# Kernel optimization log

Hardware: AMD Instinct MI355X
Metric: run time of the kernel (lower is better)

## Reference

```python
import jax, jax.numpy as jnp
from jax import lax
import numpy as np

B = 8
IN_SCALE = 9            # 1 + 2*input_window_size
S2 = IN_SCALE * IN_SCALE  # 81
MODES = 16
J = 5 * S2 + MODES      # 421
RBF = 64
HDC = 256
NCA_H = 32
NCA_STEPS = 20
MAX_T = 100.0           # max_time_step (None in source -> bug; fixed constant)


def _pool_matrix(I, O):
    # faithful AdaptiveAvgPool over dim of size I -> O (torch bin boundaries)
    M = np.zeros((O, I), np.float32)
    for o in range(O):
        s = (o * I) // O
        e = -((-(o + 1) * I) // O)
        M[o, s:e] = 1.0 / (e - s)
    return jnp.asarray(M)

POOL = _pool_matrix(J, S2)  # [81, 421]


def _meta_encoding(m_in, m_out):
    # vectorized version of the per-i loop in meta_encoding
    pos_in = m_in / MAX_T
    pos_out = m_out / MAX_T
    i = jnp.arange(MODES)
    div = jnp.power(10000.0, (2.0 * (i // 2)).astype(jnp.float32) / MODES)
    a_in = pos_in[:, None] / div[None, :]   # [B, MODES]
    a_out = pos_out[:, None] / div[None, :]
    even = (jnp.sin(a_in) + jnp.cos(a_in)) * 0.5
    odd = (jnp.cos(a_in) + jnp.sin(a_out)) * 0.5
    return jnp.where((i % 2 == 0)[None, :], even, odd)


def setup_inputs() -> dict:
    key = jax.random.key(0)
    ks = jax.random.split(key, 12)
    data_input = jax.random.uniform(ks[0], (B, 4 * IN_SCALE, IN_SCALE), jnp.float32)
    structure_input = jax.random.uniform(ks[1], (B, IN_SCALE, IN_SCALE), jnp.float32)
    meta_in = jax.random.uniform(ks[2], (B,), jnp.float32) * MAX_T
    meta_out = jax.random.uniform(ks[3], (B,), jnp.float32) * MAX_T
    # learned / fixed params
    rbf_probes = jax.random.uniform(ks[4], (RBF, J, HDC), jnp.float32) * 2.0
    compress_w = jax.random.normal(ks[5], (5, RBF), jnp.float32)
    compress_b = jnp.full((5,), 0.01, jnp.float32)
    nca_w1 = jax.random.normal(ks[6], (NCA_H, 5, 3, 3), jnp.float32) * 0.1
    nca_b1 = jnp.full((NCA_H,), 0.01, jnp.float32)
    nca_w2 = jax.random.normal(ks[7], (5, NCA_H), jnp.float32) * 0.1
    nca_b2 = jnp.full((5,), 0.01, jnp.float32)
    # sparse random +/-1 HDC projection matrix (scatter into flat zeros, as in source)
    input_dim = 5 * S2
    n_nz = input_dim * HDC
    idx = np.asarray(jax.random.randint(ks[8], (n_nz,), 0, input_dim * HDC))
    signs = np.asarray(jax.random.randint(ks[9], (n_nz,), 0, 2)).astype(np.float32) * 2.0 - 1.0
    flat = np.zeros((B * J * HDC,), np.float32)
    flat[idx] = signs
    hdc_matrix = jnp.asarray(flat.reshape(B, J, HDC))
    return {
        "data_input": data_input, "structure_input": structure_input,
        "meta_in": meta_in, "meta_out": meta_out,
        "rbf_probes": rbf_probes, "hdc_matrix": hdc_matrix,
        "compress_w": compress_w, "compress_b": compress_b,
        "nca_w1": nca_w1, "nca_b1": nca_b1, "nca_w2": nca_w2, "nca_b2": nca_b2,
    }


def _forward(data_input, structure_input, meta_in, meta_out, rbf_probes,
             hdc_matrix, compress_w, compress_b, nca_w1, nca_b1, nca_w2, nca_b2):
    pe = _meta_encoding(meta_in, meta_out)                       # [B, 16]
    data = jnp.concatenate(
        [data_input.reshape(B, -1), structure_input.reshape(B, -1), pe], axis=1)  # [B, J]
    # einsum 'bi,bjd->bjd' sums data over i and broadcasts over (j, d)
    proj = data.sum(axis=1)[:, None, None] * hdc_matrix          # [B, J, HDC]
    # broadcast RBF distance: the big memory-bound intermediate [B, RBF, J, HDC]
    dist = (rbf_probes[None, :, :, :] - proj[:, None, :, :]) ** 2
    # 1x1 conv over rbf channel dim, then tanh -> [B, 5, J, HDC]
    x = jnp.tanh(jnp.einsum('brjd,or->bojd', dist, compress_w)
                 + compress_b[None, :, None, None])

    def nca_step(x, _):
        h = lax.conv_general_dilated(x, nca_w1, (1, 1), 'SAME',
                                     dimension_numbers=('NCHW', 'OIHW', 'NCHW'))
        h = jax.nn.relu(h + nca_b1[None, :, None, None])
        dx = jnp.einsum('bhjd,oh->bojd', h, nca_w2) + nca_b2[None, :, None, None]
        return x + dx, None

    x, _ = lax.scan(nca_step, x, None, length=NCA_STEPS)
    x = jnp.tanh(x)
    # AdaptiveAvgPool2d((S2, 1)): mean over HDC, adaptive pool J -> S2
    x = jnp.einsum('bcj,oj->bco', x.mean(axis=-1), POOL)         # [B, 5, 81]
    r = x[:, 0, :].reshape(B, IN_SCALE, IN_SCALE)
    g = x[:, 1, :].reshape(B, IN_SCALE, IN_SCALE)
    b = x[:, 2, :].reshape(B, IN_SCALE, IN_SCALE)
    a = x[:, 3, :].reshape(B, IN_SCALE, IN_SCALE)
    s = x[:, 4, :].reshape(B, IN_SCALE, IN_SCALE)
    return (r, g, b, a, s)


def reference(data_input, structure_input, meta_in, meta_out, rbf_probes,
              hdc_matrix, compress_w, compress_b, nca_w1, nca_b1, nca_w2, nca_b2):
    return _forward(data_input, structure_input, meta_in, meta_out, rbf_probes,
                    hdc_matrix, compress_w, compress_b, nca_w1, nca_b1, nca_w2, nca_b2)
```

## Files before the change

### kernel.cpp

```cpp
#include <hip/hip_runtime.h>
#include <math.h>

#define NB 8
#define JJ 421
#define HDCN 256
#define PP (JJ*HDCN)
#define STEPS 20

typedef __attribute__((ext_vector_type(8))) short bf16x8;
typedef __attribute__((ext_vector_type(4))) float f32x4;
typedef __attribute__((ext_vector_type(2))) float f32x2;
typedef __attribute__((ext_vector_type(4))) unsigned int uint4v;
typedef __attribute__((ext_vector_type(2))) int int2v;
typedef unsigned short ushort;
typedef unsigned int uint;

__device__ __forceinline__ ushort f2bf(float f) {
    union { float f; uint u; } a; a.f = f;
    uint r = 0x7fffu + ((a.u >> 16) & 1u);
    return (ushort)((a.u + r) >> 16);
}
__device__ __forceinline__ uint splitpack(float x) {
    uint u = __float_as_uint(x);
    uint r = 0x7fffu + ((u >> 16) & 1u);
    uint hib = (u + r) & 0xffff0000u;
    float lo = x - __uint_as_float(hib);
    return hib | f2bf(lo);
}
__device__ __forceinline__ float unpack2(uint p) {
    return __uint_as_float(p & 0xffff0000u) + __uint_as_float(p << 16);
}
__device__ __forceinline__ float tanh_fast(float x) {
    float e = __expf(2.f * x);
    return 1.f - 2.f / (e + 1.f);
}
__device__ __forceinline__ float wave_reduce_sum(float v) {
#pragma unroll
    for (int off = 32; off > 0; off >>= 1) v += __shfl_down(v, off);
    return v;
}
__device__ __forceinline__ float red32(float d) {
#if __has_builtin(__builtin_amdgcn_permlane32_swap)
    int2v pr = __builtin_amdgcn_permlane32_swap(__float_as_int(d), __float_as_int(d), false, false);
    return __int_as_float(pr.x) + __int_as_float(pr.y);
#else
    return d + __shfl_xor(d, 32);
#endif
}

__global__ __launch_bounds__(256) void k_wprep(
    const float* __restrict__ w1, const float* __restrict__ b1,
    const float* __restrict__ w2,
    ushort* __restrict__ Pw, float* __restrict__ w2p)
{
    int t = threadIdx.x;
    for (int idx = t; idx < 3072; idx += 256) {
        int p = idx >> 10, rem = idx & 1023, oc = rem >> 5, k = rem & 31;
        int tau = k & 15;
        float v = 0.f;
        if (tau < 15) v = w1[oc * 45 + (tau / 3) * 9 + (tau % 3) * 3 + p];
        Pw[idx] = f2bf(v);
    }
    int oc = t >> 3, o = t & 7;
    float v = 0.f;
    if (o < 5) v = w2[o * 32 + oc];
    else if (o == 5) v = b1[oc];
    w2p[t] = v;
}

__global__ __launch_bounds__(128) void k_prep(
    const float* __restrict__ din, const float* __restrict__ stin,
    const float* __restrict__ m_in, const float* __restrict__ m_out,
    float* __restrict__ sbuf)
{
    int b = blockIdx.x, t = threadIdx.x;
    float acc = 0.f;
    for (int k = t; k < 324; k += 128) acc += din[b * 324 + k];
    for (int k = t; k < 81;  k += 128) acc += stin[b * 81 + k];
    if (t < 16) {
        int i = t;
        float pos_in  = m_in[b]  * 0.01f;
        float pos_out = m_out[b] * 0.01f;
        float div = powf(10000.0f, (float)(2 * (i / 2)) / 16.0f);
        float ai = pos_in / div, ao = pos_out / div;
        float v = ((i & 1) == 0) ? 0.5f * (sinf(ai) + cosf(ai))
                                 : 0.5f * (cosf(ai) + sinf(ao));
        acc += v;
    }
    __shared__ float part[2];
    float w = wave_reduce_sum(acc);
    if ((t & 63) == 0) part[t >> 6] = w;
    __syncthreads();
    if (t == 0) sbuf[b] = part[0] + part[1];
}

__global__ __launch_bounds__(128) void k_x0(
    const float* __restrict__ rbf, const float* __restrict__ hdc,
    const float* __restrict__ cw, const float* __restrict__ cb,
    const float* __restrict__ sbuf, uint* __restrict__ x0)
{
    __shared__ float wl[320];
    __shared__ float Cw[5];
    __shared__ float sb[8];
    __shared__ float cbs[5];
    int t = threadIdx.x;
    for (int k = t; k < 320; k += 128) wl[k] = cw[k];
    if (t < 8)   sb[t] = sbuf[t];
    if (t < 5)   cbs[t] = cb[t];
    __syncthreads();
    if (t < 5) { float c = 0.f; for (int r = 0; r < 64; ++r) c += wl[t * 64 + r]; Cw[t] = c; }
    __syncthreads();

    int jd = blockIdx.x * 128 + t;
    float A[5]  = {0, 0, 0, 0, 0};
    float Bv[5] = {0, 0, 0, 0, 0};
    for (int r = 0; r < 64; ++r) {
        float v  = rbf[(size_t)r * PP + jd];
        float v2 = v * v;
#pragma unroll
        for (int o = 0; o < 5; ++o) {
            float w = wl[o * 64 + r];
            A[o]  = fmaf(w, v2, A[o]);
            Bv[o] = fmaf(w, v,  Bv[o]);
        }
    }
#pragma unroll
    for (int b = 0; b < 8; ++b) {
        float p  = sb[b] * hdc[(size_t)b * PP + jd];
        float p2 = p * p;
#pragma unroll
        for (int o = 0; o < 5; ++o) {
            float val = A[o] - 2.f * p * Bv[o] + p2 * Cw[o] + cbs[o];
            x0[(size_t)(b * 5 + o) * PP + jd] = splitpack(tanh_fast(val));
        }
    }
}

__global__ __launch_bounds__(256, 3) void k_nca(
    const uint* __restrict__ xin, uint* __restrict__ xout,
    const ushort* __restrict__ Pw, const float* __restrict__ w2p,
    const float* __restrict__ b2)
{
    __shared__ uint Bs[2][258 * 16];
    __shared__ float Ds[4][5][64];

    const int t = threadIdx.x;
    const int b = blockIdx.x & 7;
    const int pj = blockIdx.x >> 3;
    const int j0 = pj * 2;
    const bool has1 = (j0 + 1) < JJ;
    const int lane = t & 63, wv = t >> 6;
    const int m = lane & 15, gq = lane >> 4;

    bf16x8 Ap[3][2];
#pragma unroll
    for (int p = 0; p < 3; ++p)
#pragma unroll
        for (int mt = 0; mt < 2; ++mt)
            Ap[p][mt] = *(const bf16x8*)(Pw + p * 1024 + (mt * 16 + m) * 32 + gq * 8);

    float w2r[2][4][5], b1r[2][4], b2r[5];
#pragma unroll
    for (int mt = 0; mt < 2; ++mt)
#pragma unroll
        for (int i = 0; i < 4; ++i) {
            int oc = mt * 16 + gq * 4 + i;
            const float* wp = w2p + oc * 8;
            f32x4 a = *(const f32x4*)wp;
            f32x2 e = *(const f32x2*)(wp + 4);
            w2r[mt][i][0] = a[0]; w2r[mt][i][1] = a[1];
            w2r[mt][i][2] = a[2]; w2r[mt][i][3] = a[3];
            w2r[mt][i][4] = e[0]; b1r[mt][i] = e[1];
        }
#pragma unroll
    for (int o = 0; o < 5; ++o) b2r[o] = b2[o];

    uint v[5][4];
    {
        const uint* xb = xin + (size_t)b * 5 * PP;
#pragma unroll
        for (int c = 0; c < 5; ++c)
#pragma unroll
            for (int rr = 0; rr < 4; ++rr) {
                int jj = j0 - 1 + rr;
                uint val = 0;
                if (jj >= 0 && jj < JJ) val = xb[(size_t)(c * JJ + jj) * HDCN + t];
                v[c][rr] = val;
            }
        const int row = t + 1;
        const int s = (row >> 1) & 3;
#pragma unroll
        for (int r = 0; r < 2; ++r) {
            if (r == 1 && !has1) break;
            uint xh[8], xl[8];
#pragma unroll
            for (int w = 0; w < 8; ++w) {
                int k0 = 2 * w, k1 = 2 * w + 1;
                uint a = (k0 < 15) ? v[k0 / 3][k0 % 3 + r] : 0u;
                uint c = (k1 < 15) ? v[k1 / 3][k1 % 3 + r] : 0u;
                xh[w] = (a >> 16) | (c & 0xffff0000u);
                xl[w] = (a & 0xffffu) | (c << 16);
            }
            uint* rb = &Bs[r][row * 16];
            *(uint4v*)(rb + ((0 ^ s) << 2)) = (uint4v){xh[0], xh[1], xh[2], xh[3]};
            *(uint4v*)(rb + ((1 ^ s) << 2)) = (uint4v){xh[4], xh[5], xh[6], xh[7]};
            *(uint4v*)(rb + ((2 ^ s) << 2)) = (uint4v){xl[0], xl[1], xl[2], xl[3]};
            *(uint4v*)(rb + ((3 ^ s) << 2)) = (uint4v){xl[4], xl[5], xl[6], xl[7]};
        }
        if (t < 4) {
            uint* zr = &Bs[t >> 1][(t & 1) ? 257 * 16 : 0];
            uint4v z = (uint4v){0, 0, 0, 0};
            ((uint4v*)zr)[0] = z; ((uint4v*)zr)[1] = z;
            ((uint4v*)zr)[2] = z; ((uint4v*)zr)[3] = z;
        }
    }
    __syncthreads();

#pragma unroll
    for (int r = 0; r < 2; ++r) {
        if (r == 1 && !has1) break;
        const int j = j0 + r;

        f32x4 acc[2][4];
#pragma unroll
        for (int mt = 0; mt < 2; ++mt)
#pragma unroll
            for (int nt = 0; nt < 4; ++nt) acc[mt][nt] = (f32x4){0.f, 0.f, 0.f, 0.f};

#pragma unroll
        for (int nt = 0; nt < 4; ++nt) {
            int px = (wv << 6) + (nt << 4) + m;
#pragma unroll
            for (int p = 0; p < 3; ++p) {
                int row = px + p;
                int s2 = (row >> 1) & 3;
                bf16x8 Bf = *(const bf16x8*)(&Bs[r][row * 16] + ((gq ^ s2) << 2));
                acc[0][nt] = __builtin_amdgcn_mfma_f32_16x16x32_bf16(Ap[p][0], Bf, acc[0][nt], 0, 0, 0);
                acc[1][nt] = __builtin_amdgcn_mfma_f32_16x16x32_bf16(Ap[p][1], Bf, acc[1][nt], 0, 0, 0);
            }
        }

#pragma unroll
        for (int nt = 0; nt < 4; ++nt) {
            float dx[5] = {0, 0, 0, 0, 0};
#pragma unroll
            for (int mt = 0; mt < 2; ++mt)
#pragma unroll
                for (int i = 0; i < 4; ++i) {
                    float h = fmaxf(acc[mt][nt][i] + b1r[mt][i], 0.f);
#pragma unroll
                    for (int o = 0; o < 5; ++o) dx[o] = fmaf(w2r[mt][i][o], h, dx[o]);
                }
#pragma unroll
            for (int o = 0; o < 5; ++o) {
                dx[o] += __shfl_xor(dx[o], 16);
                dx[o] = red32(dx[o]);
            }
            int col = (nt << 4) + m;
            if (gq == 0) {
#pragma unroll
                for (int o = 0; o < 4; ++o) Ds[wv][o][col] = dx[o];
            } else if (gq == 1) {
                Ds[wv][4][col] = dx[4];
            }
        }

        const size_t base_bj = (size_t)b * 5 * PP + (size_t)j * HDCN;
#pragma unroll
        for (int c = 0; c < 5; ++c) {
            float d = Ds[wv][c][lane];
            float xn = unpack2(v[c][r + 1]) + d + b2r[c];
            xout[base_bj + (size_t)c * PP + t] = splitpack(xn);
        }
    }
}

__global__ __launch_bounds__(256) void k_mean(
    const uint* __restrict__ x, float* __restrict__ m)
{
    int bc = blockIdx.x / 53, jblk = blockIdx.x % 53;
    int t = threadIdx.x;
    int jr = jblk * 8 + (t >> 5);
    if (jr >= JJ) return;
    const uint* p = x + (size_t)bc * PP + (size_t)jr * HDCN + (t & 31) * 8;
    uint4v u0 = *(const uint4v*)p;
    uint4v u1 = *(const uint4v*)(p + 4);
    float s = 0.f;
#pragma unroll
    for (int k = 0; k < 4; ++k) s += tanh_fast(unpack2(u0[k]));
#pragma unroll
    for (int k = 0; k < 4; ++k) s += tanh_fast(unpack2(u1[k]));
#pragma unroll
    for (int off = 16; off > 0; off >>= 1) s += __shfl_down(s, off, 32);
    if ((t & 31) == 0) m[bc * JJ + jr] = s * (1.0f / 256.0f);
}

__global__ __launch_bounds__(256) void k_out(
    const float* __restrict__ m, float* __restrict__ out)
{
    int idx = blockIdx.x * 256 + threadIdx.x;
    if (idx >= 5 * NB * 81) return;
    int c = idx / (NB * 81);
    int rem = idx % (NB * 81);
    int b = rem / 81;
    int o = rem % 81;
    int s_ = (o * JJ) / 81;
    int e_ = ((o + 1) * JJ + 80) / 81;
    float acc = 0.f;
    for (int jj = s_; jj < e_; ++jj) acc += m[(b * 5 + c) * JJ + jj];
    out[idx] = acc / (float)(e_ - s_);
}

extern "C" void kernel_launch(void* const* d_in, const int* in_sizes, int n_in,
                              void* d_out, int out_size, void* d_ws, size_t ws_size,
                              hipStream_t stream) {
    const float* data_in  = (const float*)d_in[0];
    const float* struc_in = (const float*)d_in[1];
    const float* meta_in  = (const float*)d_in[2];
    const float* meta_out = (const float*)d_in[3];
    const float* rbf      = (const float*)d_in[4];
    const float* hdc      = (const float*)d_in[5];
    const float* cw       = (const float*)d_in[6];
    const float* cb       = (const float*)d_in[7];
    const float* w1       = (const float*)d_in[8];
    const float* b1       = (const float*)d_in[9];
    const float* w2       = (const float*)d_in[10];
    const float* b2       = (const float*)d_in[11];
    float* out = (float*)d_out;

    float* ws   = (float*)d_ws;
    float* sbuf = ws;
    float* mbuf = ws + 64;
    ushort* Pw  = (ushort*)(ws + 20480);
    float* w2p  = ws + 22528;
    uint* xA = (uint*)(ws + 32768);
    uint* xB = xA + (size_t)NB * 5 * PP;

    k_wprep<<<1, 256, 0, stream>>>(w1, b1, w2, Pw, w2p);
    k_prep<<<NB, 128, 0, stream>>>(data_in, struc_in, meta_in, meta_out, sbuf);
    k_x0<<<842, 128, 0, stream>>>(rbf, hdc, cw, cb, sbuf, xA);

    for (int step = 0; step < STEPS; ++step) {
        const uint* xi = (step & 1) ? xB : xA;
        uint*       xo = (step & 1) ? xA : xB;
        k_nca<<<NB * 211, 256, 0, stream>>>(xi, xo, Pw, w2p, b2);
    }
    k_mean<<<(40 * 53), 256, 0, stream>>>(xA, mbuf);
    k_out<<<(5 * NB * 81 + 255) / 256, 256, 0, stream>>>(mbuf, out);
}
```

Before: 410.8 us.

## Split NCA conv block into single-wave blocks with per-wave halo rows

Each 256-thread k_nca block becomes four independent 64-thread blocks, each covering 64 HDC columns. The edge lanes load the neighbouring halo columns themselves, which removes the block-wide __syncthreads and the shared Ds reduction buffer. Each lane now keeps its own column's dx by selecting the nt==gq reduction result. The w2/b1 weight loads move after the MFMA loop through volatile reads to cut register pressure. The cost is redundant halo global loads done by only two divergent lanes, and four times as many small blocks to schedule.

```diff
diff --git a/kernel.cpp b/kernel.cpp
--- a/kernel.cpp
+++ b/kernel.cpp
@@ -136,20 +136,22 @@
     }
 }
 
-__global__ __launch_bounds__(256, 3) void k_nca(
+__global__ __launch_bounds__(64, 4) void k_nca(
     const uint* __restrict__ xin, uint* __restrict__ xout,
     const ushort* __restrict__ Pw, const float* __restrict__ w2p,
     const float* __restrict__ b2)
 {
-    __shared__ uint Bs[2][258 * 16];
-    __shared__ float Ds[4][5][64];
-
-    const int t = threadIdx.x;
-    const int b = blockIdx.x & 7;
-    const int pj = blockIdx.x >> 3;
+    __shared__ __align__(16) uint Bs[2][66 * 16];
+
+    const int lane = threadIdx.x;
+    const int bid = blockIdx.x;
+    const int b = bid & 7;
+    const int rem = bid >> 3;
+    const int ws_ = rem & 3;
+    const int pj = rem >> 2;
     const int j0 = pj * 2;
     const bool has1 = (j0 + 1) < JJ;
-    const int lane = t & 63, wv = t >> 6;
+    const int P = ws_ << 6;
     const int m = lane & 15, gq = lane >> 4;
 
     bf16x8 Ap[3][2];
@@ -159,36 +161,58 @@
         for (int mt = 0; mt < 2; ++mt)
             Ap[p][mt] = *(const bf16x8*)(Pw + p * 1024 + (mt * 16 + m) * 32 + gq * 8);
 
-    float w2r[2][4][5], b1r[2][4], b2r[5];
-#pragma unroll
-    for (int mt = 0; mt < 2; ++mt)
-#pragma unroll
-        for (int i = 0; i < 4; ++i) {
-            int oc = mt * 16 + gq * 4 + i;
-            const float* wp = w2p + oc * 8;
-            f32x4 a = *(const f32x4*)wp;
-            f32x2 e = *(const f32x2*)(wp + 4);
-            w2r[mt][i][0] = a[0]; w2r[mt][i][1] = a[1];
-            w2r[mt][i][2] = a[2]; w2r[mt][i][3] = a[3];
-            w2r[mt][i][4] = e[0]; b1r[mt][i] = e[1];
-        }
+    float b2r[5];
 #pragma unroll
     for (int o = 0; o < 5; ++o) b2r[o] = b2[o];
 
+    const uint* xb = xin + (size_t)b * 5 * PP;
+
     uint v[5][4];
-    {
-        const uint* xb = xin + (size_t)b * 5 * PP;
+#pragma unroll
+    for (int c = 0; c < 5; ++c)
+#pragma unroll
+        for (int rr = 0; rr < 4; ++rr) {
+            int jj = j0 - 1 + rr;
+            uint val = 0;
+            if (jj >= 0 && jj < JJ) val = xb[(size_t)(c * JJ + jj) * HDCN + P + lane];
+            v[c][rr] = val;
+        }
+
+#pragma unroll
+    for (int r = 0; r < 2; ++r) {
+        if (r == 1 && !has1) break;
+        uint xh[8], xl[8];
+#pragma unroll
+        for (int w = 0; w < 8; ++w) {
+            int k0 = 2 * w, k1 = 2 * w + 1;
+            uint a = (k0 < 15) ? v[k0 / 3][k0 % 3 + r] : 0u;
+            uint c = (k1 < 15) ? v[k1 / 3][k1 % 3 + r] : 0u;
+            xh[w] = (a >> 16) | (c & 0xffff0000u);
+            xl[w] = (a & 0xffffu) | (c << 16);
+        }
+        int rho = lane + 1;
+        int s = (rho >> 1) & 3;
+        uint* rb = &Bs[r][rho * 16];
+        *(uint4v*)(rb + ((0 ^ s) << 2)) = (uint4v){xh[0], xh[1], xh[2], xh[3]};
+        *(uint4v*)(rb + ((1 ^ s) << 2)) = (uint4v){xh[4], xh[5], xh[6], xh[7]};
+        *(uint4v*)(rb + ((2 ^ s) << 2)) = (uint4v){xl[0], xl[1], xl[2], xl[3]};
+        *(uint4v*)(rb + ((3 ^ s) << 2)) = (uint4v){xl[4], xl[5], xl[6], xl[7]};
+    }
+
+    if (lane == 0 || lane == 63) {
+        int qh = (lane == 0) ? P - 1 : P + 64;
+        int rho = (lane == 0) ? 0 : 65;
+        bool qok = (qh >= 0) && (qh < HDCN);
+        uint vh[5][4];
 #pragma unroll
         for (int c = 0; c < 5; ++c)
 #pragma unroll
             for (int rr = 0; rr < 4; ++rr) {
                 int jj = j0 - 1 + rr;
                 uint val = 0;
-                if (jj >= 0 && jj < JJ) val = xb[(size_t)(c * JJ + jj) * HDCN + t];
-                v[c][rr] = val;
-            }
-        const int row = t + 1;
-        const int s = (row >> 1) & 3;
+                if (qok && jj >= 0 && jj < JJ) val = xb[(size_t)(c * JJ + jj) * HDCN + qh];
+                vh[c][rr] = val;
+            }
 #pragma unroll
         for (int r = 0; r < 2; ++r) {
             if (r == 1 && !has1) break;
@@ -196,25 +220,19 @@
 #pragma unroll
             for (int w = 0; w < 8; ++w) {
                 int k0 = 2 * w, k1 = 2 * w + 1;
-                uint a = (k0 < 15) ? v[k0 / 3][k0 % 3 + r] : 0u;
-                uint c = (k1 < 15) ? v[k1 / 3][k1 % 3 + r] : 0u;
+                uint a = (k0 < 15) ? vh[k0 / 3][k0 % 3 + r] : 0u;
+                uint c = (k1 < 15) ? vh[k1 / 3][k1 % 3 + r] : 0u;
                 xh[w] = (a >> 16) | (c & 0xffff0000u);
                 xl[w] = (a & 0xffffu) | (c << 16);
             }
-            uint* rb = &Bs[r][row * 16];
+            int s = (rho >> 1) & 3;
+            uint* rb = &Bs[r][rho * 16];
             *(uint4v*)(rb + ((0 ^ s) << 2)) = (uint4v){xh[0], xh[1], xh[2], xh[3]};
             *(uint4v*)(rb + ((1 ^ s) << 2)) = (uint4v){xh[4], xh[5], xh[6], xh[7]};
             *(uint4v*)(rb + ((2 ^ s) << 2)) = (uint4v){xl[0], xl[1], xl[2], xl[3]};
             *(uint4v*)(rb + ((3 ^ s) << 2)) = (uint4v){xl[4], xl[5], xl[6], xl[7]};
         }
-        if (t < 4) {
-            uint* zr = &Bs[t >> 1][(t & 1) ? 257 * 16 : 0];
-            uint4v z = (uint4v){0, 0, 0, 0};
-            ((uint4v*)zr)[0] = z; ((uint4v*)zr)[1] = z;
-            ((uint4v*)zr)[2] = z; ((uint4v*)zr)[3] = z;
-        }
-    }
-    __syncthreads();
+    }
 
 #pragma unroll
     for (int r = 0; r < 2; ++r) {
@@ -229,17 +247,30 @@
 
 #pragma unroll
         for (int nt = 0; nt < 4; ++nt) {
-            int px = (wv << 6) + (nt << 4) + m;
 #pragma unroll
             for (int p = 0; p < 3; ++p) {
-                int row = px + p;
-                int s2 = (row >> 1) & 3;
-                bf16x8 Bf = *(const bf16x8*)(&Bs[r][row * 16] + ((gq ^ s2) << 2));
+                int rho = nt * 16 + m + p;
+                int s2 = (rho >> 1) & 3;
+                bf16x8 Bf = *(const bf16x8*)(&Bs[r][rho * 16] + ((gq ^ s2) << 2));
                 acc[0][nt] = __builtin_amdgcn_mfma_f32_16x16x32_bf16(Ap[p][0], Bf, acc[0][nt], 0, 0, 0);
                 acc[1][nt] = __builtin_amdgcn_mfma_f32_16x16x32_bf16(Ap[p][1], Bf, acc[1][nt], 0, 0, 0);
             }
         }
 
+        float w2r[2][4][5], b1r[2][4];
+#pragma unroll
+        for (int mt = 0; mt < 2; ++mt)
+#pragma unroll
+            for (int i = 0; i < 4; ++i) {
+                int oc = mt * 16 + gq * 4 + i;
+                f32x4 a = *(volatile const f32x4*)(w2p + oc * 8);
+                f32x2 e = *(volatile const f32x2*)(w2p + oc * 8 + 4);
+                w2r[mt][i][0] = a[0]; w2r[mt][i][1] = a[1];
+                w2r[mt][i][2] = a[2]; w2r[mt][i][3] = a[3];
+                w2r[mt][i][4] = e[0]; b1r[mt][i] = e[1];
+            }
+
+        float dxs[5] = {0, 0, 0, 0, 0};
 #pragma unroll
         for (int nt = 0; nt < 4; ++nt) {
             float dx[5] = {0, 0, 0, 0, 0};
@@ -255,22 +286,15 @@
             for (int o = 0; o < 5; ++o) {
                 dx[o] += __shfl_xor(dx[o], 16);
                 dx[o] = red32(dx[o]);
-            }
-            int col = (nt << 4) + m;
-            if (gq == 0) {
-#pragma unroll
-                for (int o = 0; o < 4; ++o) Ds[wv][o][col] = dx[o];
-            } else if (gq == 1) {
-                Ds[wv][4][col] = dx[4];
-            }
-        }
-
-        const size_t base_bj = (size_t)b * 5 * PP + (size_t)j * HDCN;
+                if (nt == gq) dxs[o] = dx[o];
+            }
+        }
+
+        const size_t base_bj = (size_t)b * 5 * PP + (size_t)j * HDCN + P + lane;
 #pragma unroll
         for (int c = 0; c < 5; ++c) {
-            float d = Ds[wv][c][lane];
-            float xn = unpack2(v[c][r + 1]) + d + b2r[c];
-            xout[base_bj + (size_t)c * PP + t] = splitpack(xn);
+            float xn = unpack2(v[c][r + 1]) + dxs[c] + b2r[c];
+            xout[base_bj + (size_t)c * PP] = splitpack(xn);
         }
     }
 }
@@ -343,7 +367,7 @@
     for (int step = 0; step < STEPS; ++step) {
         const uint* xi = (step & 1) ? xB : xA;
         uint*       xo = (step & 1) ? xA : xB;
-        k_nca<<<NB * 211, 256, 0, stream>>>(xi, xo, Pw, w2p, b2);
+        k_nca<<<NB * 211 * 4, 64, 0, stream>>>(xi, xo, Pw, w2p, b2);
     }
     k_mean<<<(40 * 53), 256, 0, stream>>>(xA, mbuf);
     k_out<<<(5 * NB * 81 + 255) / 256, 256, 0, stream>>>(mbuf, out);
```

Measured after the change: 646.8 us. 57.5% more time.

## Fuse final tanh-mean into last NCA step and drop LDS dx staging

Applied to the files above, without the earlier changes.

On the final NCA step the kernel skips writing the state to global memory and instead applies tanh, reduces each row over HDC with wave reductions and writes the mean directly, which removes the separate mean kernel and one full state write and read. The dx values are also kept in registers by selecting each lane's own column after the butterfly reduction, replacing the LDS staging buffer. This relies on a wave_reduce_sum helper and adds a block-level sync on the final step.

```diff
diff --git a/kernel.cpp b/kernel.cpp
--- a/kernel.cpp
+++ b/kernel.cpp
@@ -139,10 +139,10 @@
 __global__ __launch_bounds__(256, 3) void k_nca(
     const uint* __restrict__ xin, uint* __restrict__ xout,
     const ushort* __restrict__ Pw, const float* __restrict__ w2p,
-    const float* __restrict__ b2)
+    const float* __restrict__ b2, float* __restrict__ mbuf, int dofinal)
 {
     __shared__ uint Bs[2][258 * 16];
-    __shared__ float Ds[4][5][64];
+    __shared__ float Ms[2][5][4];
 
     const int t = threadIdx.x;
     const int b = blockIdx.x & 7;
@@ -240,6 +240,7 @@
             }
         }
 
+        float dxs[5] = {0, 0, 0, 0, 0};
 #pragma unroll
         for (int nt = 0; nt < 4; ++nt) {
             float dx[5] = {0, 0, 0, 0, 0};
@@ -255,44 +256,37 @@
             for (int o = 0; o < 5; ++o) {
                 dx[o] += __shfl_xor(dx[o], 16);
                 dx[o] = red32(dx[o]);
-            }
-            int col = (nt << 4) + m;
-            if (gq == 0) {
-#pragma unroll
-                for (int o = 0; o < 4; ++o) Ds[wv][o][col] = dx[o];
-            } else if (gq == 1) {
-                Ds[wv][4][col] = dx[4];
+                if (nt == gq) dxs[o] = dx[o];
             }
         }
 
         const size_t base_bj = (size_t)b * 5 * PP + (size_t)j * HDCN;
+        float xnv[5];
 #pragma unroll
         for (int c = 0; c < 5; ++c) {
-            float d = Ds[wv][c][lane];
-            float xn = unpack2(v[c][r + 1]) + d + b2r[c];
-            xout[base_bj + (size_t)c * PP + t] = splitpack(xn);
-        }
-    }
-}
-
-__global__ __launch_bounds__(256) void k_mean(
-    const uint* __restrict__ x, float* __restrict__ m)
-{
-    int bc = blockIdx.x / 53, jblk = blockIdx.x % 53;
-    int t = threadIdx.x;
-    int jr = jblk * 8 + (t >> 5);
-    if (jr >= JJ) return;
-    const uint* p = x + (size_t)bc * PP + (size_t)jr * HDCN + (t & 31) * 8;
-    uint4v u0 = *(const uint4v*)p;
-    uint4v u1 = *(const uint4v*)(p + 4);
-    float s = 0.f;
-#pragma unroll
-    for (int k = 0; k < 4; ++k) s += tanh_fast(unpack2(u0[k]));
-#pragma unroll
-    for (int k = 0; k < 4; ++k) s += tanh_fast(unpack2(u1[k]));
-#pragma unroll
-    for (int off = 16; off > 0; off >>= 1) s += __shfl_down(s, off, 32);
-    if ((t & 31) == 0) m[bc * JJ + jr] = s * (1.0f / 256.0f);
+            xnv[c] = unpack2(v[c][r + 1]) + dxs[c] + b2r[c];
+            if (!dofinal) xout[base_bj + (size_t)c * PP + t] = splitpack(xnv[c]);
+        }
+
+        if (dofinal) {
+#pragma unroll
+            for (int c = 0; c < 5; ++c) {
+                float s = wave_reduce_sum(tanh_fast(xnv[c]));
+                if (lane == 0) Ms[r][c][wv] = s;
+            }
+        }
+    }
+
+    if (dofinal) {
+        __syncthreads();
+        if (t < 10) {
+            int rr = t / 5, c = t % 5;
+            if (rr == 0 || has1) {
+                float s = Ms[rr][c][0] + Ms[rr][c][1] + Ms[rr][c][2] + Ms[rr][c][3];
+                mbuf[(b * 5 + c) * JJ + (j0 + rr)] = s * (1.0f / 256.0f);
+            }
+        }
+    }
 }
 
 __global__ __launch_bounds__(256) void k_out(
@@ -343,8 +337,8 @@
     for (int step = 0; step < STEPS; ++step) {
         const uint* xi = (step & 1) ? xB : xA;
         uint*       xo = (step & 1) ? xA : xB;
-        k_nca<<<NB * 211, 256, 0, stream>>>(xi, xo, Pw, w2p, b2);
-    }
-    k_mean<<<(40 * 53), 256, 0, stream>>>(xA, mbuf);
+        k_nca<<<NB * 211, 256, 0, stream>>>(xi, xo, Pw, w2p, b2, mbuf,
+                                            (step == STEPS - 1) ? 1 : 0);
+    }
     k_out<<<(5 * NB * 81 + 255) / 256, 256, 0, stream>>>(mbuf, out);
 }
```

New measurement: 403.5 us, median of 2. About the same (-1.8%).
